# Optimization experiments

Hardware: AMD Instinct MI355X
Metric: run time of the kernel (lower is better)

## Reference

```python
import jax, jax.numpy as jnp
import numpy as np

B, S, H, E = 256, 512, 256, 8
F = S // 2 + 1

def setup_inputs() -> dict:
    key = jax.random.key(0)
    ks = jax.random.split(key, 6)
    return {
        "x": jax.random.normal(ks[0], (B, S, H), dtype=jnp.float32),
        "complex_weight": jax.random.normal(ks[1], (E, F, H, 2), dtype=jnp.float32) * 0.02,
        "mlp_w": jax.random.normal(ks[2], (H, E), dtype=jnp.float32) * (1.0 / np.sqrt(H)),
        "mlp_b": jnp.zeros((E,), dtype=jnp.float32),
        "ln_gamma": jnp.ones((H,), dtype=jnp.float32),
        "ln_beta": jnp.zeros((H,), dtype=jnp.float32),
    }

def reference(x, complex_weight, mlp_w, mlp_b, ln_gamma, ln_beta):
    # x: [B, S, H]
    seq_len = x.shape[1]
    # pooling == 1 branch: rescale by number of valid (nonzero) positions
    valid_len = (x.sum(-1) != 0).sum(-1).astype(x.dtype)[:, None, None]  # [B,1,1]
    input_gate = x / (valid_len + 1e-4) * 50.0
    input_gate = jax.lax.stop_gradient(input_gate)  # trunc_gate == 1
    gate = input_gate.mean(axis=1)                  # AvgPool1d over seq -> [B,H]
    gate = jax.nn.softmax(gate @ mlp_w + mlp_b, axis=1)  # [B,E]
    # mix expert complex filters: [B,E] x [E,F,H,2] -> [B,F,H,2]
    w = jnp.einsum('be,efhc->bfhc', gate, complex_weight)
    w = w[..., 0] + 1j * w[..., 1]                  # [B,F,H] complex
    Xf = jnp.fft.rfft(x, axis=1, norm='ortho')      # [B,F,H]
    y = jnp.fft.irfft(Xf * w, n=seq_len, axis=1, norm='ortho')  # [B,S,H]
    # dropout is identity in eval mode
    h = y + x
    mean = h.mean(axis=-1, keepdims=True)
    var = h.var(axis=-1, keepdims=True)             # biased, matches torch LayerNorm
    return (h - mean) / jnp.sqrt(var + 1e-12) * ln_gamma + ln_beta
```

## Files before the change

### kernel.cpp

```cpp
#include <hip/hip_runtime.h>
#include <math.h>

namespace {

constexpr float kInv512 = 1.0f / 512.0f;

struct cpx { float x, y; };
__device__ __forceinline__ cpx cadd(cpx a, cpx b){ return {a.x+b.x, a.y+b.y}; }
__device__ __forceinline__ cpx csub(cpx a, cpx b){ return {a.x-b.x, a.y-b.y}; }
__device__ __forceinline__ cpx cmul(cpx a, cpx b){ return {a.x*b.x - a.y*b.y, a.x*b.y + a.y*b.x}; }

template<int S>
__device__ __forceinline__ cpx twmul(cpx a, cpx w){
  if (S < 0) return cpx{ a.x*w.x - a.y*w.y, a.x*w.y + a.y*w.x };
  else       return cpx{ a.x*w.x + a.y*w.y, a.y*w.x - a.x*w.y };
}

template<int S>
__device__ __forceinline__ cpx Jrot(cpx z){
  return (S < 0) ? cpx{ z.y, -z.x } : cpx{ -z.y, z.x };
}

template<int S>
__device__ __forceinline__ void dft8(cpx* A){
  const float s2 = 0.70710678118654752440f;
  cpx t0=A[0], t1=A[4], t2=A[2], t3=A[6], t4=A[1], t5=A[5], t6=A[3], t7=A[7];
  cpx b0=cadd(t0,t1), b1=csub(t0,t1), b2=cadd(t2,t3), b3=csub(t2,t3);
  cpx b4=cadd(t4,t5), b5=csub(t4,t5), b6=cadd(t6,t7), b7=csub(t6,t7);
  cpx jb3=Jrot<S>(b3), jb7=Jrot<S>(b7);
  cpx c0=cadd(b0,b2), c2=csub(b0,b2), c1=cadd(b1,jb3), c3=csub(b1,jb3);
  cpx c4=cadd(b4,b6), c6=csub(b4,b6), c5=cadd(b5,jb7), c7=csub(b5,jb7);
  cpx jc6=Jrot<S>(c6);
  cpx w5, w7;
  if (S < 0) {
    w5 = cpx{ s2*(c5.x + c5.y), s2*(c5.y - c5.x) };
    w7 = cpx{ s2*(c7.y - c7.x), -s2*(c7.x + c7.y) };
  } else {
    w5 = cpx{ s2*(c5.x - c5.y), s2*(c5.x + c5.y) };
    w7 = cpx{ -s2*(c7.x + c7.y), s2*(c7.x - c7.y) };
  }
  A[0]=cadd(c0,c4); A[4]=csub(c0,c4);
  A[2]=cadd(c2,jc6); A[6]=csub(c2,jc6);
  A[1]=cadd(c1,w5);  A[5]=csub(c1,w5);
  A[3]=cadd(c3,w7);  A[7]=csub(c3,w7);
}

__device__ __forceinline__ int slotN(int n){
  return 73*(n >> 6) + (n & 63);
}

template<int S>
__device__ void fft512(float2* zp, int l, const cpx* tw1, const cpx* tw2){
  cpx a[8];
  int k1r = l >> 3, d3 = l & 7;
  #pragma unroll
  for (int j=0;j<8;++j){
    float2 v = zp[73*j + l];
    a[j].x = v.x; a[j].y = v.y;
  }
  dft8<S>(a);
  #pragma unroll
  for (int k=1;k<8;++k) a[k] = twmul<S>(a[k], tw1[k-1]);
  #pragma unroll
  for (int k1=0;k1<8;++k1) zp[73*k1 + l] = make_float2(a[k1].x, a[k1].y);
  #pragma unroll
  for (int aa=0;aa<8;++aa){
    float2 v = zp[73*k1r + 8*aa + d3];
    a[aa].x = v.x; a[aa].y = v.y;
  }
  dft8<S>(a);
  #pragma unroll
  for (int c=1;c<8;++c) a[c] = twmul<S>(a[c], tw2[c-1]);
  #pragma unroll
  for (int c=0;c<8;++c) zp[73*k1r + 8*c + d3] = make_float2(a[c].x, a[c].y);
  #pragma unroll
  for (int b8=0;b8<8;++b8){
    float2 v = zp[73*k1r + 8*d3 + b8];
    a[b8].x = v.x; a[b8].y = v.y;
  }
  dft8<S>(a);
  int klow = k1r + 8*d3;
  #pragma unroll
  for (int d=0;d<8;++d){
    zp[73*d + klow] = make_float2(a[d].x, a[d].y);
  }
}

__global__ __launch_bounds__(256) void gate_kernel(
    const float* __restrict__ x, const float* __restrict__ mlp_w,
    const float* __restrict__ mlp_b, float* __restrict__ gate)
{
  __shared__ float tile[32][257];
  __shared__ float red[32];
  __shared__ int icnt[4];
  int b = blockIdx.x, t = threadIdx.x;
  const float* xb = x + (size_t)b * 131072;

  float colsum = 0.f;
  int cnt = 0;
  for (int ch = 0; ch < 16; ++ch){
    #pragma unroll
    for (int sr = 0; sr < 32; ++sr){
      float v = xb[(ch*32 + sr)*256 + t];
      colsum += v;
      tile[sr][t] = v;
    }
    __syncthreads();
    {
      int row = t >> 3, base = (t & 7) * 32;
      float rs = 0.f;
      #pragma unroll
      for (int j = 0; j < 32; ++j) rs += tile[row][base + j];
      rs += __shfl_xor(rs, 1);
      rs += __shfl_xor(rs, 2);
      rs += __shfl_xor(rs, 4);
      if ((t & 7) == 0) cnt += (rs != 0.f) ? 1 : 0;
    }
    __syncthreads();
  }

  for (int m=1;m<64;m<<=1) cnt += __shfl_xor(cnt, m);
  int wv = t >> 6, ln = t & 63;
  if (ln == 0) icnt[wv] = cnt;
  __syncthreads();
  float valid = (float)(icnt[0]+icnt[1]+icnt[2]+icnt[3]);
  float gi = colsum * (50.0f / ((valid + 1e-4f) * 512.0f));

  float pl[8];
  const float4* w4 = (const float4*)(mlp_w + (size_t)t*8);
  float4 wa = w4[0], wb = w4[1];
  pl[0]=gi*wa.x; pl[1]=gi*wa.y; pl[2]=gi*wa.z; pl[3]=gi*wa.w;
  pl[4]=gi*wb.x; pl[5]=gi*wb.y; pl[6]=gi*wb.z; pl[7]=gi*wb.w;
  #pragma unroll
  for (int e=0;e<8;++e){
    float v = pl[e];
    for (int m=1;m<64;m<<=1) v += __shfl_xor(v, m);
    pl[e] = v;
  }
  if (ln == 0){
    #pragma unroll
    for (int e=0;e<8;++e) red[wv*8+e] = pl[e];
  }
  __syncthreads();
  if (t < 8){
    float lg = red[0*8+t]+red[1*8+t]+red[2*8+t]+red[3*8+t] + mlp_b[t];
    float mx = lg;
    for (int m=1;m<8;m<<=1) mx = fmaxf(mx, __shfl_xor(mx, m, 8));
    float ex = expf(lg - mx);
    float sm = ex;
    for (int m=1;m<8;m<<=1) sm += __shfl_xor(sm, m, 8);
    gate[b*8 + t] = ex / sm * kInv512;
  }
}

__global__ __launch_bounds__(512) void fft_kernel(
    const float* __restrict__ x, const float* __restrict__ cw,
    const float* __restrict__ gate, float* __restrict__ out)
{
  __shared__ float2 zz[8][584];
  int t = threadIdx.x;
  int hg = blockIdx.x, b = blockIdx.y;
  int h_base = hg * 16;
  const float* xb = x + (size_t)b * 131072;
  float* ob = out + (size_t)b * 131072;

  int p = t >> 6, l = t & 63;
  float2* zp = zz[p];

  cpx tw1[7], tw2[7];
  {
    float th1 = -6.28318530717958647692f * (1.0f/512.0f) * (float)l;
    cpx w1; __sincosf(th1, &w1.y, &w1.x);
    tw1[0] = w1;
    #pragma unroll
    for (int k=1;k<7;++k) tw1[k] = cmul(tw1[k-1], w1);
    float th2 = -6.28318530717958647692f * (1.0f/64.0f) * (float)(l & 7);
    cpx w2; __sincosf(th2, &w2.y, &w2.x);
    tw2[0] = w2;
    #pragma unroll
    for (int k=1;k<7;++k) tw2[k] = cmul(tw2[k-1], w2);
  }

  float g[8];
  #pragma unroll
  for (int e=0;e<8;++e) g[e] = gate[b*8 + e];

  #pragma unroll
  for (int it=0; it<8; ++it){
    int s = it*64 + (t >> 3);
    float2 v = *(const float2*)(xb + s*256 + h_base + 2*(t & 7));
    zz[t & 7][73*it + (t >> 3)] = v;
  }
  __syncthreads();

  fft512<-1>(zp, l, tw1, tw2);
  __syncthreads();

  {
    int pc = t & 7, fq = t >> 3;
    float2* zq = zz[pc];
    int hc = h_base + 2*pc;
    #pragma unroll
    for (int it=0; it<4; ++it){
      int f = it*64 + fq;
      float2 Zf = zq[73*it + fq];
      int m = (512 - f) & 511;
      float2 Zm = zq[slotN(m)];
      float X0x = 0.5f*(Zf.x + Zm.x), X0y = 0.5f*(Zf.y - Zm.y);
      float X1x = 0.5f*(Zf.y + Zm.y), X1y = 0.5f*(Zm.x - Zf.x);
      float w0x = kInv512, w0y = 0.f, w1x = kInv512, w1y = 0.f;
      const float* cwf = cw + ((size_t)f*256 + hc)*2;
      #pragma unroll
      for (int e=0;e<8;++e){
        float4 cv = *(const float4*)(cwf + (size_t)e*131584);
        w0x += g[e]*cv.x; w0y += g[e]*cv.y;
        w1x += g[e]*cv.z; w1y += g[e]*cv.w;
      }
      float Y0x = X0x*w0x - X0y*w0y, Y0y = X0x*w0y + X0y*w0x;
      float Y1x = X1x*w1x - X1y*w1y, Y1y = X1x*w1y + X1y*w1x;
      if (f == 0){ Y0y = 0.f; Y1y = 0.f; }
      zq[73*it + fq] = make_float2(Y0x - Y1y, Y0y + Y1x);
      zq[slotN(m)]   = make_float2(Y0x + Y1y, Y1x - Y0y);
    }
    if (t < 8){
      float2* zn = zz[t];
      int hn = h_base + 2*t;
      float2 Zf = zn[292];
      float w0x = kInv512, w1x = kInv512;
      const float* cwf = cw + ((size_t)256*256 + hn)*2;
      #pragma unroll
      for (int e=0;e<8;++e){
        float4 cv = *(const float4*)(cwf + (size_t)e*131584);
        w0x += g[e]*cv.x; w1x += g[e]*cv.z;
      }
      zn[292] = make_float2(Zf.x*w0x, Zf.y*w1x);
    }
  }
  __syncthreads();

  fft512<1>(zp, l, tw1, tw2);
  __syncthreads();

  #pragma unroll
  for (int it=0; it<8; ++it){
    int s = it*64 + (t >> 3);
    float2 v = zz[t & 7][73*it + (t >> 3)];
    *(float2*)(ob + s*256 + h_base + 2*(t & 7)) = v;
  }
}

__global__ __launch_bounds__(256) void ln_kernel(
    float* __restrict__ io, const float* __restrict__ gamma,
    const float* __restrict__ beta)
{
  int t = threadIdx.x;
  int row = blockIdx.x*4 + (t >> 6);
  int ln = t & 63;
  float4* pr = (float4*)(io + (size_t)row * 256);
  float4 v = pr[ln];
  float s = (v.x+v.y)+(v.z+v.w);
  float q = (v.x*v.x + v.y*v.y) + (v.z*v.z + v.w*v.w);
  for (int m=1;m<64;m<<=1){ s += __shfl_xor(s, m); q += __shfl_xor(q, m); }
  float mean = s * (1.0f/256.0f);
  float var  = q * (1.0f/256.0f) - mean*mean;
  float rstd = rsqrtf(var + 1e-12f);
  const float4 gm = ((const float4*)gamma)[ln];
  const float4 bt = ((const float4*)beta)[ln];
  float4 o;
  o.x = (v.x - mean)*rstd*gm.x + bt.x;
  o.y = (v.y - mean)*rstd*gm.y + bt.y;
  o.z = (v.z - mean)*rstd*gm.z + bt.z;
  o.w = (v.w - mean)*rstd*gm.w + bt.w;
  pr[ln] = o;
}

}

extern "C" void kernel_launch(void* const* d_in, const int* in_sizes, int n_in,
                              void* d_out, int out_size, void* d_ws, size_t ws_size,
                              hipStream_t stream) {
  const float* x     = (const float*)d_in[0];
  const float* cw    = (const float*)d_in[1];
  const float* mlp_w = (const float*)d_in[2];
  const float* mlp_b = (const float*)d_in[3];
  const float* gamma = (const float*)d_in[4];
  const float* beta  = (const float*)d_in[5];
  float* out  = (float*)d_out;
  float* gate = (float*)d_ws;

  hipLaunchKernelGGL(gate_kernel, dim3(256), dim3(256), 0, stream,
                     x, mlp_w, mlp_b, gate);
  hipLaunchKernelGGL(fft_kernel, dim3(16, 256), dim3(512), 0, stream,
                     x, cw, gate, out);
  hipLaunchKernelGGL(ln_kernel, dim3(32768), dim3(256), 0, stream,
                     out, gamma, beta);
}
```

Measured before the change: 198.5 us.

## Process two batches per FFT block to reuse complex filter weight loads

```diff
diff --git a/kernel.cpp b/kernel.cpp
--- a/kernel.cpp
+++ b/kernel.cpp
@@ -50,39 +50,59 @@
 }
 
 template<int S>
-__device__ void fft512(float2* zp, int l, const cpx* tw1, const cpx* tw2){
-  cpx a[8];
+__device__ void fft512_dual(float2* z0, float2* z1, int l){
+  cpx a[8], b[8];
   int k1r = l >> 3, d3 = l & 7;
+  cpx tw1[7], tw2[7];
+  {
+    float th1 = -6.28318530717958647692f * (1.0f/512.0f) * (float)l;
+    cpx w1; __sincosf(th1, &w1.y, &w1.x);
+    tw1[0] = w1;
+    #pragma unroll
+    for (int k=1;k<7;++k) tw1[k] = cmul(tw1[k-1], w1);
+    float th2 = -6.28318530717958647692f * (1.0f/64.0f) * (float)d3;
+    cpx w2; __sincosf(th2, &w2.y, &w2.x);
+    tw2[0] = w2;
+    #pragma unroll
+    for (int k=1;k<7;++k) tw2[k] = cmul(tw2[k-1], w2);
+  }
   #pragma unroll
   for (int j=0;j<8;++j){
-    float2 v = zp[73*j + l];
-    a[j].x = v.x; a[j].y = v.y;
-  }
-  dft8<S>(a);
-  #pragma unroll
-  for (int k=1;k<8;++k) a[k] = twmul<S>(a[k], tw1[k-1]);
-  #pragma unroll
-  for (int k1=0;k1<8;++k1) zp[73*k1 + l] = make_float2(a[k1].x, a[k1].y);
+    float2 v0 = z0[73*j + l]; a[j].x = v0.x; a[j].y = v0.y;
+    float2 v1 = z1[73*j + l]; b[j].x = v1.x; b[j].y = v1.y;
+  }
+  dft8<S>(a); dft8<S>(b);
+  #pragma unroll
+  for (int k=1;k<8;++k){ a[k] = twmul<S>(a[k], tw1[k-1]); b[k] = twmul<S>(b[k], tw1[k-1]); }
+  #pragma unroll
+  for (int k1=0;k1<8;++k1){
+    z0[73*k1 + l] = make_float2(a[k1].x, a[k1].y);
+    z1[73*k1 + l] = make_float2(b[k1].x, b[k1].y);
+  }
   #pragma unroll
   for (int aa=0;aa<8;++aa){
-    float2 v = zp[73*k1r + 8*aa + d3];
-    a[aa].x = v.x; a[aa].y = v.y;
-  }
-  dft8<S>(a);
-  #pragma unroll
-  for (int c=1;c<8;++c) a[c] = twmul<S>(a[c], tw2[c-1]);
-  #pragma unroll
-  for (int c=0;c<8;++c) zp[73*k1r + 8*c + d3] = make_float2(a[c].x, a[c].y);
+    float2 v0 = z0[73*k1r + 8*aa + d3]; a[aa].x = v0.x; a[aa].y = v0.y;
+    float2 v1 = z1[73*k1r + 8*aa + d3]; b[aa].x = v1.x; b[aa].y = v1.y;
+  }
+  dft8<S>(a); dft8<S>(b);
+  #pragma unroll
+  for (int c=1;c<8;++c){ a[c] = twmul<S>(a[c], tw2[c-1]); b[c] = twmul<S>(b[c], tw2[c-1]); }
+  #pragma unroll
+  for (int c=0;c<8;++c){
+    z0[73*k1r + 8*c + d3] = make_float2(a[c].x, a[c].y);
+    z1[73*k1r + 8*c + d3] = make_float2(b[c].x, b[c].y);
+  }
   #pragma unroll
   for (int b8=0;b8<8;++b8){
-    float2 v = zp[73*k1r + 8*d3 + b8];
-    a[b8].x = v.x; a[b8].y = v.y;
-  }
-  dft8<S>(a);
+    float2 v0 = z0[73*k1r + 8*d3 + b8]; a[b8].x = v0.x; a[b8].y = v0.y;
+    float2 v1 = z1[73*k1r + 8*d3 + b8]; b[b8].x = v1.x; b[b8].y = v1.y;
+  }
+  dft8<S>(a); dft8<S>(b);
   int klow = k1r + 8*d3;
   #pragma unroll
   for (int d=0;d<8;++d){
-    zp[73*d + klow] = make_float2(a[d].x, a[d].y);
+    z0[73*d + klow] = make_float2(a[d].x, a[d].y);
+    z1[73*d + klow] = make_float2(b[d].x, b[d].y);
   }
 }
 
@@ -157,95 +177,112 @@
     const float* __restrict__ x, const float* __restrict__ cw,
     const float* __restrict__ gate, float* __restrict__ out)
 {
-  __shared__ float2 zz[8][584];
+  __shared__ float2 zz[16][584];
   int t = threadIdx.x;
-  int hg = blockIdx.x, b = blockIdx.y;
+  int hg = blockIdx.x, bp = blockIdx.y;
+  int b0 = 2*bp;
   int h_base = hg * 16;
-  const float* xb = x + (size_t)b * 131072;
-  float* ob = out + (size_t)b * 131072;
-
-  int p = t >> 6, l = t & 63;
-  float2* zp = zz[p];
-
-  cpx tw1[7], tw2[7];
-  {
-    float th1 = -6.28318530717958647692f * (1.0f/512.0f) * (float)l;
-    cpx w1; __sincosf(th1, &w1.y, &w1.x);
-    tw1[0] = w1;
-    #pragma unroll
-    for (int k=1;k<7;++k) tw1[k] = cmul(tw1[k-1], w1);
-    float th2 = -6.28318530717958647692f * (1.0f/64.0f) * (float)(l & 7);
-    cpx w2; __sincosf(th2, &w2.y, &w2.x);
-    tw2[0] = w2;
-    #pragma unroll
-    for (int k=1;k<7;++k) tw2[k] = cmul(tw2[k-1], w2);
-  }
-
-  float g[8];
-  #pragma unroll
-  for (int e=0;e<8;++e) g[e] = gate[b*8 + e];
+  const float* xb0 = x + (size_t)b0 * 131072;
+  const float* xb1 = xb0 + 131072;
+  float* ob0 = out + (size_t)b0 * 131072;
+  float* ob1 = ob0 + 131072;
+
+  float g0[8], g1[8];
+  #pragma unroll
+  for (int e=0;e<8;++e){ g0[e] = gate[b0*8 + e]; g1[e] = gate[b0*8 + 8 + e]; }
 
   #pragma unroll
   for (int it=0; it<8; ++it){
     int s = it*64 + (t >> 3);
-    float2 v = *(const float2*)(xb + s*256 + h_base + 2*(t & 7));
-    zz[t & 7][73*it + (t >> 3)] = v;
-  }
-  __syncthreads();
-
-  fft512<-1>(zp, l, tw1, tw2);
+    int pr = t & 7, sl = 73*it + (t >> 3);
+    float2 v0 = *(const float2*)(xb0 + s*256 + h_base + 2*pr);
+    float2 v1 = *(const float2*)(xb1 + s*256 + h_base + 2*pr);
+    zz[pr][sl] = v0;
+    zz[8 + pr][sl] = v1;
+  }
+  __syncthreads();
+
+  int p = t >> 6, l = t & 63;
+  float2* zp0 = zz[p];
+  float2* zp1 = zz[8 + p];
+
+  fft512_dual<-1>(zp0, zp1, l);
   __syncthreads();
 
   {
     int pc = t & 7, fq = t >> 3;
-    float2* zq = zz[pc];
+    float2* zq0 = zz[pc];
+    float2* zq1 = zz[8 + pc];
     int hc = h_base + 2*pc;
     #pragma unroll
     for (int it=0; it<4; ++it){
       int f = it*64 + fq;
-      float2 Zf = zq[73*it + fq];
+      int sf = 73*it + fq;
       int m = (512 - f) & 511;
-      float2 Zm = zq[slotN(m)];
-      float X0x = 0.5f*(Zf.x + Zm.x), X0y = 0.5f*(Zf.y - Zm.y);
-      float X1x = 0.5f*(Zf.y + Zm.y), X1y = 0.5f*(Zm.x - Zf.x);
-      float w0x = kInv512, w0y = 0.f, w1x = kInv512, w1y = 0.f;
+      int sm = slotN(m);
+      float2 Zf0 = zq0[sf], Zm0 = zq0[sm];
+      float2 Zf1 = zq1[sf], Zm1 = zq1[sm];
+      float w00x = kInv512, w00y = 0.f, w01x = kInv512, w01y = 0.f;
+      float w10x = kInv512, w10y = 0.f, w11x = kInv512, w11y = 0.f;
       const float* cwf = cw + ((size_t)f*256 + hc)*2;
       #pragma unroll
       for (int e=0;e<8;++e){
         float4 cv = *(const float4*)(cwf + (size_t)e*131584);
-        w0x += g[e]*cv.x; w0y += g[e]*cv.y;
-        w1x += g[e]*cv.z; w1y += g[e]*cv.w;
+        w00x += g0[e]*cv.x; w00y += g0[e]*cv.y;
+        w01x += g0[e]*cv.z; w01y += g0[e]*cv.w;
+        w10x += g1[e]*cv.x; w10y += g1[e]*cv.y;
+        w11x += g1[e]*cv.z; w11y += g1[e]*cv.w;
       }
-      float Y0x = X0x*w0x - X0y*w0y, Y0y = X0x*w0y + X0y*w0x;
-      float Y1x = X1x*w1x - X1y*w1y, Y1y = X1x*w1y + X1y*w1x;
-      if (f == 0){ Y0y = 0.f; Y1y = 0.f; }
-      zq[73*it + fq] = make_float2(Y0x - Y1y, Y0y + Y1x);
-      zq[slotN(m)]   = make_float2(Y0x + Y1y, Y1x - Y0y);
+      {
+        float X0x = 0.5f*(Zf0.x + Zm0.x), X0y = 0.5f*(Zf0.y - Zm0.y);
+        float X1x = 0.5f*(Zf0.y + Zm0.y), X1y = 0.5f*(Zm0.x - Zf0.x);
+        float Y0x = X0x*w00x - X0y*w00y, Y0y = X0x*w00y + X0y*w00x;
+        float Y1x = X1x*w01x - X1y*w01y, Y1y = X1x*w01y + X1y*w01x;
+        if (f == 0){ Y0y = 0.f; Y1y = 0.f; }
+        zq0[sf] = make_float2(Y0x - Y1y, Y0y + Y1x);
+        zq0[sm] = make_float2(Y0x + Y1y, Y1x - Y0y);
+      }
+      {
+        float X0x = 0.5f*(Zf1.x + Zm1.x), X0y = 0.5f*(Zf1.y - Zm1.y);
+        float X1x = 0.5f*(Zf1.y + Zm1.y), X1y = 0.5f*(Zm1.x - Zf1.x);
+        float Y0x = X0x*w10x - X0y*w10y, Y0y = X0x*w10y + X0y*w10x;
+        float Y1x = X1x*w11x - X1y*w11y, Y1y = X1x*w11y + X1y*w11x;
+        if (f == 0){ Y0y = 0.f; Y1y = 0.f; }
+        zq1[sf] = make_float2(Y0x - Y1y, Y0y + Y1x);
+        zq1[sm] = make_float2(Y0x + Y1y, Y1x - Y0y);
+      }
     }
     if (t < 8){
-      float2* zn = zz[t];
+      float2* zn0 = zz[t];
+      float2* zn1 = zz[8 + t];
       int hn = h_base + 2*t;
-      float2 Zf = zn[292];
-      float w0x = kInv512, w1x = kInv512;
+      float2 Zf0 = zn0[292];
+      float2 Zf1 = zn1[292];
+      float w00x = kInv512, w01x = kInv512, w10x = kInv512, w11x = kInv512;
       const float* cwf = cw + ((size_t)256*256 + hn)*2;
       #pragma unroll
       for (int e=0;e<8;++e){
         float4 cv = *(const float4*)(cwf + (size_t)e*131584);
-        w0x += g[e]*cv.x; w1x += g[e]*cv.z;
+        w00x += g0[e]*cv.x; w01x += g0[e]*cv.z;
+        w10x += g1[e]*cv.x; w11x += g1[e]*cv.z;
       }
-      zn[292] = make_float2(Zf.x*w0x, Zf.y*w1x);
+      zn0[292] = make_float2(Zf0.x*w00x, Zf0.y*w01x);
+      zn1[292] = make_float2(Zf1.x*w10x, Zf1.y*w11x);
     }
   }
   __syncthreads();
 
-  fft512<1>(zp, l, tw1, tw2);
+  fft512_dual<1>(zp0, zp1, l);
   __syncthreads();
 
   #pragma unroll
   for (int it=0; it<8; ++it){
     int s = it*64 + (t >> 3);
-    float2 v = zz[t & 7][73*it + (t >> 3)];
-    *(float2*)(ob + s*256 + h_base + 2*(t & 7)) = v;
+    int pr = t & 7, sl = 73*it + (t >> 3);
+    float2 v0 = zz[pr][sl];
+    float2 v1 = zz[8 + pr][sl];
+    *(float2*)(ob0 + s*256 + h_base + 2*pr) = v0;
+    *(float2*)(ob1 + s*256 + h_base + 2*pr) = v1;
   }
 }
 
@@ -290,7 +327,7 @@
 
   hipLaunchKernelGGL(gate_kernel, dim3(256), dim3(256), 0, stream,
                      x, mlp_w, mlp_b, gate);
-  hipLaunchKernelGGL(fft_kernel, dim3(16, 256), dim3(512), 0, stream,
+  hipLaunchKernelGGL(fft_kernel, dim3(16, 128), dim3(512), 0, stream,
                      x, cw, gate, out);
   hipLaunchKernelGGL(ln_kernel, dim3(32768), dim3(256), 0, stream,
                      out, gamma, beta);
```

After: 228.0 us. 14.9% more time.

## Fuse spectral filter into register-resident FFT and pre-transpose complex weights

Applied to the files above, without the earlier changes.

```diff
diff --git a/kernel.cpp b/kernel.cpp
--- a/kernel.cpp
+++ b/kernel.cpp
@@ -9,12 +9,6 @@
 __device__ __forceinline__ cpx cadd(cpx a, cpx b){ return {a.x+b.x, a.y+b.y}; }
 __device__ __forceinline__ cpx csub(cpx a, cpx b){ return {a.x-b.x, a.y-b.y}; }
 __device__ __forceinline__ cpx cmul(cpx a, cpx b){ return {a.x*b.x - a.y*b.y, a.x*b.y + a.y*b.x}; }
-
-template<int S>
-__device__ __forceinline__ cpx twmul(cpx a, cpx w){
-  if (S < 0) return cpx{ a.x*w.x - a.y*w.y, a.x*w.y + a.y*w.x };
-  else       return cpx{ a.x*w.x + a.y*w.y, a.y*w.x - a.x*w.y };
-}
 
 template<int S>
 __device__ __forceinline__ cpx Jrot(cpx z){
@@ -49,40 +43,21 @@
   return 73*(n >> 6) + (n & 63);
 }
 
-template<int S>
-__device__ void fft512(float2* zp, int l, const cpx* tw1, const cpx* tw2){
-  cpx a[8];
-  int k1r = l >> 3, d3 = l & 7;
-  #pragma unroll
-  for (int j=0;j<8;++j){
-    float2 v = zp[73*j + l];
-    a[j].x = v.x; a[j].y = v.y;
-  }
-  dft8<S>(a);
-  #pragma unroll
-  for (int k=1;k<8;++k) a[k] = twmul<S>(a[k], tw1[k-1]);
-  #pragma unroll
-  for (int k1=0;k1<8;++k1) zp[73*k1 + l] = make_float2(a[k1].x, a[k1].y);
-  #pragma unroll
-  for (int aa=0;aa<8;++aa){
-    float2 v = zp[73*k1r + 8*aa + d3];
-    a[aa].x = v.x; a[aa].y = v.y;
-  }
-  dft8<S>(a);
-  #pragma unroll
-  for (int c=1;c<8;++c) a[c] = twmul<S>(a[c], tw2[c-1]);
-  #pragma unroll
-  for (int c=0;c<8;++c) zp[73*k1r + 8*c + d3] = make_float2(a[c].x, a[c].y);
-  #pragma unroll
-  for (int b8=0;b8<8;++b8){
-    float2 v = zp[73*k1r + 8*d3 + b8];
-    a[b8].x = v.x; a[b8].y = v.y;
-  }
-  dft8<S>(a);
-  int klow = k1r + 8*d3;
-  #pragma unroll
-  for (int d=0;d<8;++d){
-    zp[73*d + klow] = make_float2(a[d].x, a[d].y);
+__device__ __forceinline__ float bperm(int addr, float v){
+  return __int_as_float(__builtin_amdgcn_ds_bpermute(addr, __float_as_int(v)));
+}
+
+__global__ __launch_bounds__(128) void cwt_kernel(
+    const float* __restrict__ cw, float* __restrict__ cwT)
+{
+  int e = blockIdx.x, fg = blockIdx.y, pr = threadIdx.x;
+  const float4* src = (const float4*)cw;
+  float4* dst = (float4*)cwT;
+  int nf = (fg == 15) ? 17 : 16;
+  int f0 = fg * 16;
+  for (int i = 0; i < nf; ++i){
+    int f = f0 + i;
+    dst[(e*128 + pr)*257 + f] = src[(e*257 + f)*128 + pr];
   }
 }
 
@@ -153,7 +128,178 @@
   }
 }
 
-__global__ __launch_bounds__(512) void fft_kernel(
+__global__ __launch_bounds__(512) void fft_kernel2(
+    const float* __restrict__ x, const float* __restrict__ cwT,
+    const float* __restrict__ gate, float* __restrict__ out)
+{
+  __shared__ float2 zz[8][584];
+  int t = threadIdx.x;
+  int hg = blockIdx.x, b = blockIdx.y;
+  int h_base = hg * 16;
+  const float* xb = x + (size_t)b * 131072;
+  float* ob = out + (size_t)b * 131072;
+
+  int p = t >> 6, l = t & 63;
+  float2* zp = zz[p];
+  int k1r = l >> 3, d3 = l & 7;
+  int klow = k1r + 8*d3;
+  int mk = (64 - klow) & 63;
+  int lmir = (mk >> 3) + 8*(mk & 7);
+  int ad = lmir << 2;
+
+  float g[8];
+  #pragma unroll
+  for (int e=0;e<8;++e) g[e] = gate[b*8 + e];
+
+  #pragma unroll
+  for (int it=0; it<8; ++it){
+    float2 v = *(const float2*)(xb + (it*64 + (t>>3))*256 + h_base + 2*(t & 7));
+    zz[t & 7][73*it + (t >> 3)] = v;
+  }
+
+  int pg = hg*8 + p;
+  const float4* cT = (const float4*)cwT;
+  float4 acc1[4];
+  #pragma unroll
+  for (int j=0;j<4;++j) acc1[j] = make_float4(kInv512, 0.f, kInv512, 0.f);
+  #pragma unroll
+  for (int e=0;e<8;++e){
+    int base = (e*128 + pg)*257 + klow;
+    float ge = g[e];
+    #pragma unroll
+    for (int j=0;j<4;++j){
+      float4 c = cT[base + 64*j];
+      acc1[j].x += ge*c.x; acc1[j].y += ge*c.y;
+      acc1[j].z += ge*c.z; acc1[j].w += ge*c.w;
+    }
+  }
+  float4 acc2[4];
+  #pragma unroll
+  for (int j=0;j<4;++j){
+    acc2[j].x = bperm(ad, acc1[j].x);
+    acc2[j].y = bperm(ad, acc1[j].y);
+    acc2[j].z = bperm(ad, acc1[j].z);
+    acc2[j].w = bperm(ad, acc1[j].w);
+  }
+  if (l == 0){
+    acc2[0] = acc1[1]; acc2[1] = acc1[2]; acc2[2] = acc1[3];
+    float4 a256 = make_float4(kInv512, 0.f, kInv512, 0.f);
+    #pragma unroll
+    for (int e=0;e<8;++e){
+      float4 c = cT[(e*128 + pg)*257 + 256];
+      a256.x += g[e]*c.x; a256.y += g[e]*c.y;
+      a256.z += g[e]*c.z; a256.w += g[e]*c.w;
+    }
+    acc2[3] = a256;
+  }
+  __syncthreads();
+
+  cpx a[8];
+  {
+    cpx tw1[7], tw2[7];
+    float th1 = -6.28318530717958647692f * (1.0f/512.0f) * (float)l;
+    cpx w1; __sincosf(th1, &w1.y, &w1.x);
+    tw1[0] = w1;
+    #pragma unroll
+    for (int k=1;k<7;++k) tw1[k] = cmul(tw1[k-1], w1);
+    float th2 = -6.28318530717958647692f * (1.0f/64.0f) * (float)d3;
+    cpx w2; __sincosf(th2, &w2.y, &w2.x);
+    tw2[0] = w2;
+    #pragma unroll
+    for (int k=1;k<7;++k) tw2[k] = cmul(tw2[k-1], w2);
+
+    #pragma unroll
+    for (int j=0;j<8;++j){ float2 v = zp[73*j + l]; a[j] = {v.x, v.y}; }
+    dft8<-1>(a);
+    #pragma unroll
+    for (int k=1;k<8;++k) a[k] = cmul(a[k], tw1[k-1]);
+    #pragma unroll
+    for (int k1=0;k1<8;++k1) zp[73*k1 + l] = make_float2(a[k1].x, a[k1].y);
+
+    #pragma unroll
+    for (int aa=0;aa<8;++aa){ float2 v = zp[73*k1r + 8*aa + d3]; a[aa] = {v.x, v.y}; }
+    dft8<-1>(a);
+    #pragma unroll
+    for (int c=1;c<8;++c) a[c] = cmul(a[c], tw2[c-1]);
+    #pragma unroll
+    for (int c=0;c<8;++c) zp[73*k1r + 8*c + d3] = make_float2(a[c].x, a[c].y);
+
+    #pragma unroll
+    for (int b8=0;b8<8;++b8){ float2 v = zp[73*k1r + 8*d3 + b8]; a[b8] = {v.x, v.y}; }
+    dft8<-1>(a);
+  }
+
+  cpx Zm[8];
+  #pragma unroll
+  for (int d=0;d<8;++d){
+    Zm[d].x = bperm(ad, a[7-d].x);
+    Zm[d].y = bperm(ad, a[7-d].y);
+  }
+  if (l == 0){
+    #pragma unroll
+    for (int d=0;d<8;++d) Zm[d] = a[(8-d)&7];
+  }
+  cpx q[8];
+  #pragma unroll
+  for (int d=0;d<8;++d){
+    float4 w = (d < 4) ? acc1[d] : acc2[7-d];
+    float sg = (d < 4) ? 1.f : -1.f;
+    float w0x = w.x, w0y = sg*w.y, w1x = w.z, w1y = sg*w.w;
+    float X0x = 0.5f*(a[d].x + Zm[d].x), X0y = 0.5f*(a[d].y - Zm[d].y);
+    float X1x = 0.5f*(a[d].y + Zm[d].y), X1y = 0.5f*(Zm[d].x - a[d].x);
+    float Y0x = X0x*w0x - X0y*w0y, Y0y = X0x*w0y + X0y*w0x;
+    float Y1x = X1x*w1x - X1y*w1y, Y1y = X1x*w1y + X1y*w1x;
+    q[d] = { Y0x - Y1y, Y0y + Y1x };
+  }
+  if (l == 0){
+    q[0] = { a[0].x*acc1[0].x, a[0].y*acc1[0].z };
+    q[4] = { a[4].x*acc2[3].x, a[4].y*acc2[3].z };
+  }
+
+  {
+    int v = klow, vk1r = d3, vd3 = k1r;
+    cpx tw1[7], tw2[7];
+    float th1 = 6.28318530717958647692f * (1.0f/512.0f) * (float)v;
+    cpx w1; __sincosf(th1, &w1.y, &w1.x);
+    tw1[0] = w1;
+    #pragma unroll
+    for (int k=1;k<7;++k) tw1[k] = cmul(tw1[k-1], w1);
+    float th2 = 6.28318530717958647692f * (1.0f/64.0f) * (float)vd3;
+    cpx w2; __sincosf(th2, &w2.y, &w2.x);
+    tw2[0] = w2;
+    #pragma unroll
+    for (int k=1;k<7;++k) tw2[k] = cmul(tw2[k-1], w2);
+
+    dft8<1>(q);
+    #pragma unroll
+    for (int k=1;k<8;++k) q[k] = cmul(q[k], tw1[k-1]);
+    #pragma unroll
+    for (int k1=0;k1<8;++k1) zp[73*k1 + v] = make_float2(q[k1].x, q[k1].y);
+
+    #pragma unroll
+    for (int aa=0;aa<8;++aa){ float2 vv = zp[73*vk1r + 8*aa + vd3]; q[aa] = {vv.x, vv.y}; }
+    dft8<1>(q);
+    #pragma unroll
+    for (int c=1;c<8;++c) q[c] = cmul(q[c], tw2[c-1]);
+    #pragma unroll
+    for (int c=0;c<8;++c) zp[73*vk1r + 8*c + vd3] = make_float2(q[c].x, q[c].y);
+
+    #pragma unroll
+    for (int b8=0;b8<8;++b8){ float2 vv = zp[73*vk1r + 8*vd3 + b8]; q[b8] = {vv.x, vv.y}; }
+    dft8<1>(q);
+    #pragma unroll
+    for (int d=0;d<8;++d) zp[73*d + l] = make_float2(q[d].x, q[d].y);
+  }
+  __syncthreads();
+
+  #pragma unroll
+  for (int it=0; it<8; ++it){
+    float2 v = zz[t & 7][73*it + (t >> 3)];
+    *(float2*)(ob + (it*64 + (t>>3))*256 + h_base + 2*(t & 7)) = v;
+  }
+}
+
+__global__ __launch_bounds__(512) void fft_kernel_fb(
     const float* __restrict__ x, const float* __restrict__ cw,
     const float* __restrict__ gate, float* __restrict__ out)
 {
@@ -166,6 +312,7 @@
 
   int p = t >> 6, l = t & 63;
   float2* zp = zz[p];
+  int k1r = l >> 3, d3 = l & 7;
 
   cpx tw1[7], tw2[7];
   {
@@ -174,7 +321,7 @@
     tw1[0] = w1;
     #pragma unroll
     for (int k=1;k<7;++k) tw1[k] = cmul(tw1[k-1], w1);
-    float th2 = -6.28318530717958647692f * (1.0f/64.0f) * (float)(l & 7);
+    float th2 = -6.28318530717958647692f * (1.0f/64.0f) * (float)d3;
     cpx w2; __sincosf(th2, &w2.y, &w2.x);
     tw2[0] = w2;
     #pragma unroll
@@ -193,7 +340,29 @@
   }
   __syncthreads();
 
-  fft512<-1>(zp, l, tw1, tw2);
+  {
+    cpx a[8];
+    #pragma unroll
+    for (int j=0;j<8;++j){ float2 v = zp[73*j + l]; a[j] = {v.x, v.y}; }
+    dft8<-1>(a);
+    #pragma unroll
+    for (int k=1;k<8;++k) a[k] = cmul(a[k], tw1[k-1]);
+    #pragma unroll
+    for (int k1=0;k1<8;++k1) zp[73*k1 + l] = make_float2(a[k1].x, a[k1].y);
+    #pragma unroll
+    for (int aa=0;aa<8;++aa){ float2 v = zp[73*k1r + 8*aa + d3]; a[aa] = {v.x, v.y}; }
+    dft8<-1>(a);
+    #pragma unroll
+    for (int c=1;c<8;++c) a[c] = cmul(a[c], tw2[c-1]);
+    #pragma unroll
+    for (int c=0;c<8;++c) zp[73*k1r + 8*c + d3] = make_float2(a[c].x, a[c].y);
+    #pragma unroll
+    for (int b8=0;b8<8;++b8){ float2 v = zp[73*k1r + 8*d3 + b8]; a[b8] = {v.x, v.y}; }
+    dft8<-1>(a);
+    int klow = k1r + 8*d3;
+    #pragma unroll
+    for (int d=0;d<8;++d) zp[73*d + klow] = make_float2(a[d].x, a[d].y);
+  }
   __syncthreads();
 
   {
@@ -238,7 +407,29 @@
   }
   __syncthreads();
 
-  fft512<1>(zp, l, tw1, tw2);
+  {
+    cpx a[8];
+    #pragma unroll
+    for (int j=0;j<8;++j){ float2 v = zp[73*j + l]; a[j] = {v.x, v.y}; }
+    dft8<1>(a);
+    #pragma unroll
+    for (int k=1;k<8;++k){ cpx w = tw1[k-1]; a[k] = cpx{ a[k].x*w.x + a[k].y*w.y, a[k].y*w.x - a[k].x*w.y }; }
+    #pragma unroll
+    for (int k1=0;k1<8;++k1) zp[73*k1 + l] = make_float2(a[k1].x, a[k1].y);
+    #pragma unroll
+    for (int aa=0;aa<8;++aa){ float2 v = zp[73*k1r + 8*aa + d3]; a[aa] = {v.x, v.y}; }
+    dft8<1>(a);
+    #pragma unroll
+    for (int c=1;c<8;++c){ cpx w = tw2[c-1]; a[c] = cpx{ a[c].x*w.x + a[c].y*w.y, a[c].y*w.x - a[c].x*w.y }; }
+    #pragma unroll
+    for (int c=0;c<8;++c) zp[73*k1r + 8*c + d3] = make_float2(a[c].x, a[c].y);
+    #pragma unroll
+    for (int b8=0;b8<8;++b8){ float2 v = zp[73*k1r + 8*d3 + b8]; a[b8] = {v.x, v.y}; }
+    dft8<1>(a);
+    int klow = k1r + 8*d3;
+    #pragma unroll
+    for (int d=0;d<8;++d) zp[73*d + klow] = make_float2(a[d].x, a[d].y);
+  }
   __syncthreads();
 
   #pragma unroll
@@ -290,8 +481,18 @@
 
   hipLaunchKernelGGL(gate_kernel, dim3(256), dim3(256), 0, stream,
                      x, mlp_w, mlp_b, gate);
-  hipLaunchKernelGGL(fft_kernel, dim3(16, 256), dim3(512), 0, stream,
-                     x, cw, gate, out);
+
+  const size_t cwT_bytes = (size_t)8*128*257*4*sizeof(float);
+  if (ws_size >= 8192 + cwT_bytes){
+    float* cwT = (float*)((char*)d_ws + 8192);
+    hipLaunchKernelGGL(cwt_kernel, dim3(8,16), dim3(128), 0, stream, cw, cwT);
+    hipLaunchKernelGGL(fft_kernel2, dim3(16, 256), dim3(512), 0, stream,
+                       x, cwT, gate, out);
+  } else {
+    hipLaunchKernelGGL(fft_kernel_fb, dim3(16, 256), dim3(512), 0, stream,
+                       x, cw, gate, out);
+  }
+
   hipLaunchKernelGGL(ln_kernel, dim3(32768), dim3(256), 0, stream,
                      out, gamma, beta);
 }
```

New measurement: 314.2 us. 58.3% more time.

## Split gate reduction across four blocks per batch and inline FFT stages

Applied to the files above, without the earlier changes.

```diff
diff --git a/kernel.cpp b/kernel.cpp
--- a/kernel.cpp
+++ b/kernel.cpp
@@ -9,12 +9,6 @@
 __device__ __forceinline__ cpx cadd(cpx a, cpx b){ return {a.x+b.x, a.y+b.y}; }
 __device__ __forceinline__ cpx csub(cpx a, cpx b){ return {a.x-b.x, a.y-b.y}; }
 __device__ __forceinline__ cpx cmul(cpx a, cpx b){ return {a.x*b.x - a.y*b.y, a.x*b.y + a.y*b.x}; }
-
-template<int S>
-__device__ __forceinline__ cpx twmul(cpx a, cpx w){
-  if (S < 0) return cpx{ a.x*w.x - a.y*w.y, a.x*w.y + a.y*w.x };
-  else       return cpx{ a.x*w.x + a.y*w.y, a.y*w.x - a.x*w.y };
-}
 
 template<int S>
 __device__ __forceinline__ cpx Jrot(cpx z){
@@ -49,56 +43,20 @@
   return 73*(n >> 6) + (n & 63);
 }
 
-template<int S>
-__device__ void fft512(float2* zp, int l, const cpx* tw1, const cpx* tw2){
-  cpx a[8];
-  int k1r = l >> 3, d3 = l & 7;
-  #pragma unroll
-  for (int j=0;j<8;++j){
-    float2 v = zp[73*j + l];
-    a[j].x = v.x; a[j].y = v.y;
-  }
-  dft8<S>(a);
-  #pragma unroll
-  for (int k=1;k<8;++k) a[k] = twmul<S>(a[k], tw1[k-1]);
-  #pragma unroll
-  for (int k1=0;k1<8;++k1) zp[73*k1 + l] = make_float2(a[k1].x, a[k1].y);
-  #pragma unroll
-  for (int aa=0;aa<8;++aa){
-    float2 v = zp[73*k1r + 8*aa + d3];
-    a[aa].x = v.x; a[aa].y = v.y;
-  }
-  dft8<S>(a);
-  #pragma unroll
-  for (int c=1;c<8;++c) a[c] = twmul<S>(a[c], tw2[c-1]);
-  #pragma unroll
-  for (int c=0;c<8;++c) zp[73*k1r + 8*c + d3] = make_float2(a[c].x, a[c].y);
-  #pragma unroll
-  for (int b8=0;b8<8;++b8){
-    float2 v = zp[73*k1r + 8*d3 + b8];
-    a[b8].x = v.x; a[b8].y = v.y;
-  }
-  dft8<S>(a);
-  int klow = k1r + 8*d3;
-  #pragma unroll
-  for (int d=0;d<8;++d){
-    zp[73*d + klow] = make_float2(a[d].x, a[d].y);
-  }
-}
-
-__global__ __launch_bounds__(256) void gate_kernel(
+__global__ __launch_bounds__(256) void gate1_kernel(
     const float* __restrict__ x, const float* __restrict__ mlp_w,
-    const float* __restrict__ mlp_b, float* __restrict__ gate)
+    float* __restrict__ ws)
 {
   __shared__ float tile[32][257];
   __shared__ float red[32];
   __shared__ int icnt[4];
-  int b = blockIdx.x, t = threadIdx.x;
-  const float* xb = x + (size_t)b * 131072;
+  int blk = blockIdx.x, t = threadIdx.x;
+  int b = blk >> 2, q = blk & 3;
+  const float* xb = x + (size_t)b * 131072 + (size_t)q * 32768;
 
   float colsum = 0.f;
   int cnt = 0;
-  for (int ch = 0; ch < 16; ++ch){
+  for (int ch = 0; ch < 4; ++ch){
     #pragma unroll
     for (int sr = 0; sr < 32; ++sr){
       float v = xb[(ch*32 + sr)*256 + t];
@@ -122,15 +80,12 @@
   for (int m=1;m<64;m<<=1) cnt += __shfl_xor(cnt, m);
   int wv = t >> 6, ln = t & 63;
   if (ln == 0) icnt[wv] = cnt;
-  __syncthreads();
-  float valid = (float)(icnt[0]+icnt[1]+icnt[2]+icnt[3]);
-  float gi = colsum * (50.0f / ((valid + 1e-4f) * 512.0f));
 
   float pl[8];
   const float4* w4 = (const float4*)(mlp_w + (size_t)t*8);
   float4 wa = w4[0], wb = w4[1];
-  pl[0]=gi*wa.x; pl[1]=gi*wa.y; pl[2]=gi*wa.z; pl[3]=gi*wa.w;
-  pl[4]=gi*wb.x; pl[5]=gi*wb.y; pl[6]=gi*wb.z; pl[7]=gi*wb.w;
+  pl[0]=colsum*wa.x; pl[1]=colsum*wa.y; pl[2]=colsum*wa.z; pl[3]=colsum*wa.w;
+  pl[4]=colsum*wb.x; pl[5]=colsum*wb.y; pl[6]=colsum*wb.z; pl[7]=colsum*wb.w;
   #pragma unroll
   for (int e=0;e<8;++e){
     float v = pl[e];
@@ -143,14 +98,37 @@
   }
   __syncthreads();
   if (t < 8){
-    float lg = red[0*8+t]+red[1*8+t]+red[2*8+t]+red[3*8+t] + mlp_b[t];
-    float mx = lg;
-    for (int m=1;m<8;m<<=1) mx = fmaxf(mx, __shfl_xor(mx, m, 8));
-    float ex = expf(lg - mx);
-    float sm = ex;
-    for (int m=1;m<8;m<<=1) sm += __shfl_xor(sm, m, 8);
-    gate[b*8 + t] = ex / sm * kInv512;
-  }
+    ws[blk*12 + t] = red[0*8+t]+red[1*8+t]+red[2*8+t]+red[3*8+t];
+  }
+  if (t == 8){
+    ws[blk*12 + 8] = (float)(icnt[0]+icnt[1]+icnt[2]+icnt[3]);
+  }
+}
+
+__global__ __launch_bounds__(256) void gate2_kernel(
+    const float* __restrict__ ws, const float* __restrict__ mlp_b,
+    float* __restrict__ gate)
+{
+  int b = threadIdx.x;
+  float raw[8] = {0,0,0,0,0,0,0,0};
+  float valid = 0.f;
+  #pragma unroll
+  for (int q=0;q<4;++q){
+    int base = (b*4 + q)*12;
+    #pragma unroll
+    for (int e=0;e<8;++e) raw[e] += ws[base + e];
+    valid += ws[base + 8];
+  }
+  float scale = 50.0f / ((valid + 1e-4f) * 512.0f);
+  float lg[8], mx = -1e30f;
+  #pragma unroll
+  for (int e=0;e<8;++e){ lg[e] = raw[e]*scale + mlp_b[e]; mx = fmaxf(mx, lg[e]); }
+  float sm = 0.f;
+  #pragma unroll
+  for (int e=0;e<8;++e){ lg[e] = expf(lg[e] - mx); sm += lg[e]; }
+  float inv = kInv512 / sm;
+  #pragma unroll
+  for (int e=0;e<8;++e) gate[b*8 + e] = lg[e] * inv;
 }
 
 __global__ __launch_bounds__(512) void fft_kernel(
@@ -166,6 +144,7 @@
 
   int p = t >> 6, l = t & 63;
   float2* zp = zz[p];
+  int k1r = l >> 3, d3 = l & 7;
 
   cpx tw1[7], tw2[7];
   {
@@ -174,7 +153,7 @@
     tw1[0] = w1;
     #pragma unroll
     for (int k=1;k<7;++k) tw1[k] = cmul(tw1[k-1], w1);
-    float th2 = -6.28318530717958647692f * (1.0f/64.0f) * (float)(l & 7);
+    float th2 = -6.28318530717958647692f * (1.0f/64.0f) * (float)d3;
     cpx w2; __sincosf(th2, &w2.y, &w2.x);
     tw2[0] = w2;
     #pragma unroll
@@ -193,7 +172,29 @@
   }
   __syncthreads();
 
-  fft512<-1>(zp, l, tw1, tw2);
+  {
+    cpx a[8];
+    #pragma unroll
+    for (int j=0;j<8;++j){ float2 v = zp[73*j + l]; a[j] = {v.x, v.y}; }
+    dft8<-1>(a);
+    #pragma unroll
+    for (int k=1;k<8;++k) a[k] = cmul(a[k], tw1[k-1]);
+    #pragma unroll
+    for (int k1=0;k1<8;++k1) zp[73*k1 + l] = make_float2(a[k1].x, a[k1].y);
+    #pragma unroll
+    for (int aa=0;aa<8;++aa){ float2 v = zp[73*k1r + 8*aa + d3]; a[aa] = {v.x, v.y}; }
+    dft8<-1>(a);
+    #pragma unroll
+    for (int c=1;c<8;++c) a[c] = cmul(a[c], tw2[c-1]);
+    #pragma unroll
+    for (int c=0;c<8;++c) zp[73*k1r + 8*c + d3] = make_float2(a[c].x, a[c].y);
+    #pragma unroll
+    for (int b8=0;b8<8;++b8){ float2 v = zp[73*k1r + 8*d3 + b8]; a[b8] = {v.x, v.y}; }
+    dft8<-1>(a);
+    int klow = k1r + 8*d3;
+    #pragma unroll
+    for (int d=0;d<8;++d) zp[73*d + klow] = make_float2(a[d].x, a[d].y);
+  }
   __syncthreads();
 
   {
@@ -238,7 +239,29 @@
   }
   __syncthreads();
 
-  fft512<1>(zp, l, tw1, tw2);
+  {
+    cpx a[8];
+    #pragma unroll
+    for (int j=0;j<8;++j){ float2 v = zp[73*j + l]; a[j] = {v.x, v.y}; }
+    dft8<1>(a);
+    #pragma unroll
+    for (int k=1;k<8;++k){ cpx w = tw1[k-1]; a[k] = cpx{ a[k].x*w.x + a[k].y*w.y, a[k].y*w.x - a[k].x*w.y }; }
+    #pragma unroll
+    for (int k1=0;k1<8;++k1) zp[73*k1 + l] = make_float2(a[k1].x, a[k1].y);
+    #pragma unroll
+    for (int aa=0;aa<8;++aa){ float2 v = zp[73*k1r + 8*aa + d3]; a[aa] = {v.x, v.y}; }
+    dft8<1>(a);
+    #pragma unroll
+    for (int c=1;c<8;++c){ cpx w = tw2[c-1]; a[c] = cpx{ a[c].x*w.x + a[c].y*w.y, a[c].y*w.x - a[c].x*w.y }; }
+    #pragma unroll
+    for (int c=0;c<8;++c) zp[73*k1r + 8*c + d3] = make_float2(a[c].x, a[c].y);
+    #pragma unroll
+    for (int b8=0;b8<8;++b8){ float2 v = zp[73*k1r + 8*d3 + b8]; a[b8] = {v.x, v.y}; }
+    dft8<1>(a);
+    int klow = k1r + 8*d3;
+    #pragma unroll
+    for (int d=0;d<8;++d) zp[73*d + klow] = make_float2(a[d].x, a[d].y);
+  }
   __syncthreads();
 
   #pragma unroll
@@ -286,10 +309,13 @@
   const float* gamma = (const float*)d_in[4];
   const float* beta  = (const float*)d_in[5];
   float* out  = (float*)d_out;
-  float* gate = (float*)d_ws;
-
-  hipLaunchKernelGGL(gate_kernel, dim3(256), dim3(256), 0, stream,
-                     x, mlp_w, mlp_b, gate);
+  float* part = (float*)d_ws;
+  float* gate = part + 1024*12;
+
+  hipLaunchKernelGGL(gate1_kernel, dim3(1024), dim3(256), 0, stream,
+                     x, mlp_w, part);
+  hipLaunchKernelGGL(gate2_kernel, dim3(1), dim3(256), 0, stream,
+                     part, mlp_b, gate);
   hipLaunchKernelGGL(fft_kernel, dim3(16, 256), dim3(512), 0, stream,
                      x, cw, gate, out);
   hipLaunchKernelGGL(ln_kernel, dim3(32768), dim3(256), 0, stream,
```

Result: faster. 186.1 us (-6.2%).
